# Optimization experiments

Hardware: AMD Instinct MI355X
Metric: run time of the kernel (lower is better)

Reference implementation:

```python
import jax, jax.numpy as jnp
import numpy as np

N = 50000
E = 800000
IN_DIM = 128
HID = 128
OUT_DIM = 64


def _xavier(key, fan_in, fan_out):
    # matches nn.init.xavier_uniform_ on a (out, in) weight
    limit = float(np.sqrt(6.0 / (fan_in + fan_out)))
    return jax.random.uniform(key, (fan_in, fan_out), jnp.float32, -limit, limit)


def setup_inputs() -> dict:
    key = jax.random.key(0)
    ks = jax.random.split(key, 7)
    X = jax.random.normal(ks[0], (N, IN_DIM), jnp.float32)
    edge_row = jax.random.randint(ks[1], (E,), 0, N, jnp.int32)
    edge_col = jax.random.randint(ks[2], (E,), 0, N, jnp.int32)
    edge_weight = jax.random.uniform(ks[3], (E,), jnp.float32)
    W1 = _xavier(ks[4], IN_DIM, HID)
    b1 = jnp.zeros((HID,), jnp.float32)
    W2 = _xavier(ks[5], HID, HID)
    b2 = jnp.zeros((HID,), jnp.float32)
    W3 = _xavier(ks[6], HID, OUT_DIM)
    b3 = jnp.zeros((OUT_DIM,), jnp.float32)
    return {"X": X, "edge_row": edge_row, "edge_col": edge_col,
            "edge_weight": edge_weight,
            "W1": W1, "b1": b1, "W2": W2, "b2": b2, "W3": W3, "b3": b3}


def _spmm(edge_row, edge_col, edge_weight, H):
    # sparse A @ H via gather + segment_sum (COO SpMM)
    msgs = edge_weight[:, None] * H[edge_col]  # [E, d]
    return jax.ops.segment_sum(msgs, edge_row, num_segments=N)


def reference(X, edge_row, edge_col, edge_weight, W1, b1, W2, b2, W3, b3):
    # layer 1: SpMM -> linear -> relu (dropout disabled: eval mode)
    h = _spmm(edge_row, edge_col, edge_weight, X)
    h = jax.nn.relu(h @ W1 + b1)
    # layer 2
    h = _spmm(edge_row, edge_col, edge_weight, h)
    h = jax.nn.relu(h @ W2 + b2)
    # layer 3 (no activation)
    h = _spmm(edge_row, edge_col, edge_weight, h)
    return h @ W3 + b3
```

## Files before the change

kernel.cpp:

```cpp
#include <hip/hip_runtime.h>
#include <hip/hip_fp16.h>


typedef unsigned int uint32;
typedef _Float16 f16x8 __attribute__((ext_vector_type(8)));
using f32x4 = __attribute__((ext_vector_type(4))) float;

static constexpr int BCAP = 3072;

static __device__ __forceinline__ unsigned short f2h(float x) {
    return __builtin_bit_cast(unsigned short, (_Float16)x);
}
static __device__ __forceinline__ __half2 u2h2(uint32 u) {
    return __builtin_bit_cast(__half2, u);
}

__global__ __launch_bounds__(256) void prep_kernel(const float* __restrict__ W1,
                                                   const float* __restrict__ W2,
                                                   const float* __restrict__ W3,
                                                   unsigned short* __restrict__ Wt1,
                                                   unsigned short* __restrict__ Wt2,
                                                   unsigned short* __restrict__ Wt3,
                                                   int* __restrict__ bcur, int nb) {
    int gid = blockIdx.x * 256 + threadIdx.x;
    if (gid < nb) bcur[gid] = 0;
    if (gid < 16384) {
        Wt1[gid] = f2h(W1[(gid & 127) * 128 + (gid >> 7)]);
    } else if (gid < 32768) {
        int g = gid - 16384;
        Wt2[g] = f2h(W2[(g & 127) * 128 + (g >> 7)]);
    } else if (gid < 40960) {
        int g = gid - 32768;
        Wt3[g] = f2h(W3[(g & 127) * 64 + (g >> 7)]);
    }
}

__global__ __launch_bounds__(256) void bucket_scatter_kernel(const int* __restrict__ erow,
                                                             const int* __restrict__ ecol,
                                                             const float* __restrict__ ew,
                                                             int* __restrict__ bcur,
                                                             int2* __restrict__ ebuf, int e) {
    __shared__ int hist[512];
    __shared__ int psc[256];
    __shared__ int fixup[512];
    __shared__ int2 stage[4096];
    int t = threadIdx.x;
    hist[t] = 0; hist[t + 256] = 0;
    __syncthreads();
    int base = blockIdx.x * 4096;
    int4 rows[4];
#pragma unroll
    for (int j = 0; j < 4; j++) {
        int idx = base + j * 1024 + t * 4;
        int4 r = make_int4(-1, -1, -1, -1);
        if (idx + 3 < e) {
            r = *reinterpret_cast<const int4*>(&erow[idx]);
        } else {
            if (idx < e)     r.x = erow[idx];
            if (idx + 1 < e) r.y = erow[idx + 1];
            if (idx + 2 < e) r.z = erow[idx + 2];
            if (idx + 3 < e) r.w = erow[idx + 3];
        }
        rows[j] = r;
        if (r.x >= 0) atomicAdd(&hist[r.x >> 7], 1);
        if (r.y >= 0) atomicAdd(&hist[r.y >> 7], 1);
        if (r.z >= 0) atomicAdd(&hist[r.z >> 7], 1);
        if (r.w >= 0) atomicAdd(&hist[r.w >> 7], 1);
    }
    __syncthreads();
    int c0 = hist[2 * t], c1 = hist[2 * t + 1];
    int s = c0 + c1;
    psc[t] = s;
    __syncthreads();
    for (int off = 1; off < 256; off <<= 1) {
        int u = (t >= off) ? psc[t - off] : 0;
        __syncthreads();
        psc[t] += u;
        __syncthreads();
    }
    int lo0 = psc[t] - s;
    int lo1 = lo0 + c0;
    if (c0) fixup[2 * t]     = 2 * t * BCAP       + atomicAdd(&bcur[2 * t], c0)     - lo0;
    if (c1) fixup[2 * t + 1] = (2 * t + 1) * BCAP + atomicAdd(&bcur[2 * t + 1], c1) - lo1;
    __syncthreads();
    hist[2 * t] = lo0; hist[2 * t + 1] = lo1;
    __syncthreads();
#pragma unroll
    for (int j = 0; j < 4; j++) {
        int idx = base + j * 1024 + t * 4;
        int4 r = rows[j];
        int4 c = make_int4(0, 0, 0, 0);
        float4 w = make_float4(0.f, 0.f, 0.f, 0.f);
        if (idx + 3 < e) {
            c = *reinterpret_cast<const int4*>(&ecol[idx]);
            w = *reinterpret_cast<const float4*>(&ew[idx]);
        } else {
            if (idx < e)     { c.x = ecol[idx];     w.x = ew[idx]; }
            if (idx + 1 < e) { c.y = ecol[idx + 1]; w.y = ew[idx + 1]; }
            if (idx + 2 < e) { c.z = ecol[idx + 2]; w.z = ew[idx + 2]; }
            if (idx + 3 < e) { c.w = ecol[idx + 3]; w.w = ew[idx + 3]; }
        }
        if (r.x >= 0) { int b = r.x >> 7; int sl = atomicAdd(&hist[b], 1);
            stage[sl] = make_int2((b << 23) | ((r.x & 127) << 16) | c.x, (int)f2h(w.x)); }
        if (r.y >= 0) { int b = r.y >> 7; int sl = atomicAdd(&hist[b], 1);
            stage[sl] = make_int2((b << 23) | ((r.y & 127) << 16) | c.y, (int)f2h(w.y)); }
        if (r.z >= 0) { int b = r.z >> 7; int sl = atomicAdd(&hist[b], 1);
            stage[sl] = make_int2((b << 23) | ((r.z & 127) << 16) | c.z, (int)f2h(w.z)); }
        if (r.w >= 0) { int b = r.w >> 7; int sl = atomicAdd(&hist[b], 1);
            stage[sl] = make_int2((b << 23) | ((r.w & 127) << 16) | c.w, (int)f2h(w.w)); }
    }
    __syncthreads();
    int ecnt = min(4096, e - base);
    for (int i = t; i < ecnt; i += 256) {
        int2 v = stage[i];
        int b = ((unsigned)v.x) >> 23;
        int gpos = fixup[b] + i;
        if (gpos - b * BCAP < BCAP) ebuf[gpos] = v;
    }
}

__global__ __launch_bounds__(256) void bucket_sort_kernel(const int* __restrict__ bcur,
                                                          const int2* __restrict__ ebuf,
                                                          int* __restrict__ ecsr,
                                                          int* __restrict__ row_ptr,
                                                          int n, int nb) {
    __shared__ int sc[512];
    __shared__ int2 stage[BCAP];
    __shared__ int sorted[BCAP];
    __shared__ int rc[128], rs[128], c2[128];
    int b = blockIdx.x;
    int t = threadIdx.x;
    sc[t]       = (t < nb)       ? min(bcur[t], BCAP)       : 0;
    sc[t + 256] = (t + 256 < nb) ? min(bcur[t + 256], BCAP) : 0;
    if (t < 128) { rc[t] = 0; c2[t] = 0; }
    __syncthreads();
    for (int off = 1; off < 512; off <<= 1) {
        int a0 = (t >= off) ? sc[t - off] : 0;
        int a1 = (t + 256 >= off) ? sc[t + 256 - off] : 0;
        __syncthreads();
        sc[t] += a0; sc[t + 256] += a1;
        __syncthreads();
    }
    int off_b = (b == 0) ? 0 : sc[b - 1];
    int cnt = sc[b] - off_b;
    if (b == 0 && t == 0) row_ptr[n] = sc[nb - 1];
    for (int i = t; i < cnt; i += 256) {
        int2 v = ebuf[b * BCAP + i];
        stage[i] = v;
        atomicAdd(&rc[(v.x >> 16) & 127], 1);
    }
    __syncthreads();
    if (t < 128) rs[t] = rc[t];
    __syncthreads();
    for (int o = 1; o < 128; o <<= 1) {
        int u = 0;
        if (t < 128 && t >= o) u = rs[t - o];
        __syncthreads();
        if (t < 128) rs[t] += u;
        __syncthreads();
    }
    if (t < 128) {
        int gr = b * 128 + t;
        if (gr < n) row_ptr[gr] = off_b + rs[t] - rc[t];
    }
    __syncthreads();
    for (int i = t; i < cnt; i += 256) {
        int2 v = stage[i];
        int r = (v.x >> 16) & 127;
        int pos = rs[r] - rc[r] + atomicAdd(&c2[r], 1);
        sorted[pos] = (v.y << 16) | (v.x & 0xFFFF);
    }
    __syncthreads();
    for (int i = t; i < cnt; i += 256) ecsr[off_b + i] = sorted[i];
}

template <bool AF32, int NOUT>
__global__ __launch_bounds__(256) void gemm_mfma_kernel(const void* __restrict__ Ap,
                                                        const unsigned short* __restrict__ Wt,
                                                        unsigned short* __restrict__ Zh, int n) {
    constexpr int CT = NOUT / 16;
    int wave = threadIdx.x >> 6;
    int lane = threadIdx.x & 63;
    int m0 = blockIdx.x * 64 + wave * 16;
    int r = lane & 15;
    int g = lane >> 4;
    int arow = min(m0 + r, n - 1);
    f32x4 acc[CT] = {};
#pragma unroll
    for (int kt = 0; kt < 4; kt++) {
        int k0 = kt * 32 + g * 8;
        f16x8 a;
        if constexpr (AF32) {
            const float* A = (const float*)Ap;
            float4 x0 = *reinterpret_cast<const float4*>(&A[(size_t)arow * 128 + k0]);
            float4 x1 = *reinterpret_cast<const float4*>(&A[(size_t)arow * 128 + k0 + 4]);
            a[0] = (_Float16)x0.x; a[1] = (_Float16)x0.y;
            a[2] = (_Float16)x0.z; a[3] = (_Float16)x0.w;
            a[4] = (_Float16)x1.x; a[5] = (_Float16)x1.y;
            a[6] = (_Float16)x1.z; a[7] = (_Float16)x1.w;
        } else {
            const unsigned short* A = (const unsigned short*)Ap;
            a = *reinterpret_cast<const f16x8*>(&A[(size_t)arow * 128 + k0]);
        }
#pragma unroll
        for (int c = 0; c < CT; c++) {
            f16x8 bb = *reinterpret_cast<const f16x8*>(&Wt[(size_t)(c * 16 + r) * 128 + k0]);
            acc[c] = __builtin_amdgcn_mfma_f32_16x16x32_f16(a, bb, acc[c], 0, 0, 0);
        }
    }
#pragma unroll
    for (int c = 0; c < CT; c++) {
#pragma unroll
        for (int rr = 0; rr < 4; rr++) {
            int row = m0 + g * 4 + rr;
            if (row < n) Zh[(size_t)row * NOUT + c * 16 + r] = f2h(acc[c][rr]);
        }
    }
}

__global__ __launch_bounds__(256) void spmm128_kernel(const int* __restrict__ row_ptr,
                                                      const int* __restrict__ ecw,
                                                      const unsigned short* __restrict__ Zh,
                                                      const float* __restrict__ bias,
                                                      unsigned short* __restrict__ Hh, int n) {
    int row = (blockIdx.x * 256 + threadIdx.x) >> 6;
    int lane = threadIdx.x & 63;
    if (row >= n) return;
    int beg = row_ptr[row], end = row_ptr[row + 1];
    int deg = end - beg;
    const int grp = lane >> 4;
    const int gl  = lane & 15;
    __half2 acc[4];
#pragma unroll
    for (int j = 0; j < 4; j++) acc[j] = u2h2(0u);
    for (int wb = 0; wb < deg; wb += 64) {
        int rem = deg - wb;
        int mv = (lane < rem) ? ecw[beg + wb + lane] : 0;
        int nc = (min(rem, 64) + 3) >> 2;
        for (int c0 = 0; c0 < nc; c0 += 4) {
            int v0 = __shfl(mv, (c0 + 0) * 4 + grp, 64);
            int v1 = __shfl(mv, (c0 + 1) * 4 + grp, 64);
            int v2 = __shfl(mv, (c0 + 2) * 4 + grp, 64);
            int v3 = __shfl(mv, (c0 + 3) * 4 + grp, 64);
            uint4 z0 = *reinterpret_cast<const uint4*>(&Zh[((size_t)(uint32)(v0 & 0xFFFF) << 7) + (gl << 3)]);
            uint4 z1 = *reinterpret_cast<const uint4*>(&Zh[((size_t)(uint32)(v1 & 0xFFFF) << 7) + (gl << 3)]);
            uint4 z2 = *reinterpret_cast<const uint4*>(&Zh[((size_t)(uint32)(v2 & 0xFFFF) << 7) + (gl << 3)]);
            uint4 z3 = *reinterpret_cast<const uint4*>(&Zh[((size_t)(uint32)(v3 & 0xFFFF) << 7) + (gl << 3)]);
            uint32 s0 = (uint32)v0 >> 16; s0 |= s0 << 16;
            uint32 s1 = (uint32)v1 >> 16; s1 |= s1 << 16;
            uint32 s2 = (uint32)v2 >> 16; s2 |= s2 << 16;
            uint32 s3 = (uint32)v3 >> 16; s3 |= s3 << 16;
            __half2 w0 = u2h2(s0), w1 = u2h2(s1), w2 = u2h2(s2), w3 = u2h2(s3);
            acc[0] = __hfma2(w0, u2h2(z0.x), acc[0]);
            acc[1] = __hfma2(w0, u2h2(z0.y), acc[1]);
            acc[2] = __hfma2(w0, u2h2(z0.z), acc[2]);
            acc[3] = __hfma2(w0, u2h2(z0.w), acc[3]);
            acc[0] = __hfma2(w1, u2h2(z1.x), acc[0]);
            acc[1] = __hfma2(w1, u2h2(z1.y), acc[1]);
            acc[2] = __hfma2(w1, u2h2(z1.z), acc[2]);
            acc[3] = __hfma2(w1, u2h2(z1.w), acc[3]);
            acc[0] = __hfma2(w2, u2h2(z2.x), acc[0]);
            acc[1] = __hfma2(w2, u2h2(z2.y), acc[1]);
            acc[2] = __hfma2(w2, u2h2(z2.z), acc[2]);
            acc[3] = __hfma2(w2, u2h2(z2.w), acc[3]);
            acc[0] = __hfma2(w3, u2h2(z3.x), acc[0]);
            acc[1] = __hfma2(w3, u2h2(z3.y), acc[1]);
            acc[2] = __hfma2(w3, u2h2(z3.z), acc[2]);
            acc[3] = __hfma2(w3, u2h2(z3.w), acc[3]);
        }
    }
#pragma unroll
    for (int j = 0; j < 4; j++) {
        int u = __builtin_bit_cast(int, acc[j]);
        acc[j] = __hadd2(acc[j], __builtin_bit_cast(__half2, __shfl_xor(u, 16, 64)));
        u = __builtin_bit_cast(int, acc[j]);
        acc[j] = __hadd2(acc[j], __builtin_bit_cast(__half2, __shfl_xor(u, 32, 64)));
    }
    if (lane < 16) {
        int d0 = gl << 3;
        float4 b0 = *reinterpret_cast<const float4*>(&bias[d0]);
        float4 b1 = *reinterpret_cast<const float4*>(&bias[d0 + 4]);
        float2 f0 = __half22float2(acc[0]);
        float2 f1 = __half22float2(acc[1]);
        float2 f2 = __half22float2(acc[2]);
        float2 f3 = __half22float2(acc[3]);
        float v0 = fmaxf(f0.x + b0.x, 0.f), v1 = fmaxf(f0.y + b0.y, 0.f);
        float v2 = fmaxf(f1.x + b0.z, 0.f), v3 = fmaxf(f1.y + b0.w, 0.f);
        float v4 = fmaxf(f2.x + b1.x, 0.f), v5 = fmaxf(f2.y + b1.y, 0.f);
        float v6 = fmaxf(f3.x + b1.z, 0.f), v7 = fmaxf(f3.y + b1.w, 0.f);
        uint4 pk;
        pk.x = (uint32)f2h(v0) | ((uint32)f2h(v1) << 16);
        pk.y = (uint32)f2h(v2) | ((uint32)f2h(v3) << 16);
        pk.z = (uint32)f2h(v4) | ((uint32)f2h(v5) << 16);
        pk.w = (uint32)f2h(v6) | ((uint32)f2h(v7) << 16);
        *reinterpret_cast<uint4*>(&Hh[(size_t)row * 128 + d0]) = pk;
    }
}

__global__ __launch_bounds__(256) void spmm64_kernel(const int* __restrict__ row_ptr,
                                                     const int* __restrict__ ecw,
                                                     const unsigned short* __restrict__ Zh,
                                                     const float* __restrict__ bias,
                                                     float* __restrict__ out, int n) {
    int row = (blockIdx.x * 256 + threadIdx.x) >> 6;
    int lane = threadIdx.x & 63;
    if (row >= n) return;
    int beg = row_ptr[row], end = row_ptr[row + 1];
    int deg = end - beg;
    const int grp = lane >> 4;
    const int gl  = lane & 15;
    __half2 acc[2];
    acc[0] = u2h2(0u); acc[1] = u2h2(0u);
    for (int wb = 0; wb < deg; wb += 64) {
        int rem = deg - wb;
        int mv = (lane < rem) ? ecw[beg + wb + lane] : 0;
        int nc = (min(rem, 64) + 3) >> 2;
        for (int c0 = 0; c0 < nc; c0 += 4) {
            int v0 = __shfl(mv, (c0 + 0) * 4 + grp, 64);
            int v1 = __shfl(mv, (c0 + 1) * 4 + grp, 64);
            int v2 = __shfl(mv, (c0 + 2) * 4 + grp, 64);
            int v3 = __shfl(mv, (c0 + 3) * 4 + grp, 64);
            uint2 z0 = *reinterpret_cast<const uint2*>(&Zh[((size_t)(uint32)(v0 & 0xFFFF) << 6) + (gl << 2)]);
            uint2 z1 = *reinterpret_cast<const uint2*>(&Zh[((size_t)(uint32)(v1 & 0xFFFF) << 6) + (gl << 2)]);
            uint2 z2 = *reinterpret_cast<const uint2*>(&Zh[((size_t)(uint32)(v2 & 0xFFFF) << 6) + (gl << 2)]);
            uint2 z3 = *reinterpret_cast<const uint2*>(&Zh[((size_t)(uint32)(v3 & 0xFFFF) << 6) + (gl << 2)]);
            uint32 s0 = (uint32)v0 >> 16; s0 |= s0 << 16;
            uint32 s1 = (uint32)v1 >> 16; s1 |= s1 << 16;
            uint32 s2 = (uint32)v2 >> 16; s2 |= s2 << 16;
            uint32 s3 = (uint32)v3 >> 16; s3 |= s3 << 16;
            acc[0] = __hfma2(u2h2(s0), u2h2(z0.x), acc[0]);
            acc[1] = __hfma2(u2h2(s0), u2h2(z0.y), acc[1]);
            acc[0] = __hfma2(u2h2(s1), u2h2(z1.x), acc[0]);
            acc[1] = __hfma2(u2h2(s1), u2h2(z1.y), acc[1]);
            acc[0] = __hfma2(u2h2(s2), u2h2(z2.x), acc[0]);
            acc[1] = __hfma2(u2h2(s2), u2h2(z2.y), acc[1]);
            acc[0] = __hfma2(u2h2(s3), u2h2(z3.x), acc[0]);
            acc[1] = __hfma2(u2h2(s3), u2h2(z3.y), acc[1]);
        }
    }
#pragma unroll
    for (int j = 0; j < 2; j++) {
        int u = __builtin_bit_cast(int, acc[j]);
        acc[j] = __hadd2(acc[j], __builtin_bit_cast(__half2, __shfl_xor(u, 16, 64)));
        u = __builtin_bit_cast(int, acc[j]);
        acc[j] = __hadd2(acc[j], __builtin_bit_cast(__half2, __shfl_xor(u, 32, 64)));
    }
    if (lane < 16) {
        int d0 = gl << 2;
        float4 b0 = *reinterpret_cast<const float4*>(&bias[d0]);
        float2 f0 = __half22float2(acc[0]);
        float2 f1 = __half22float2(acc[1]);
        float4 v = make_float4(f0.x + b0.x, f0.y + b0.y, f1.x + b0.z, f1.y + b0.w);
        *reinterpret_cast<float4*>(&out[(size_t)row * 64 + d0]) = v;
    }
}

extern "C" void kernel_launch(void* const* d_in, const int* in_sizes, int n_in,
                              void* d_out, int out_size, void* d_ws, size_t ws_size,
                              hipStream_t stream) {
    const float* X    = (const float*)d_in[0];
    const int*   erow = (const int*)d_in[1];
    const int*   ecol = (const int*)d_in[2];
    const float* ew   = (const float*)d_in[3];
    const float* W1   = (const float*)d_in[4];
    const float* b1   = (const float*)d_in[5];
    const float* W2   = (const float*)d_in[6];
    const float* b2   = (const float*)d_in[7];
    const float* W3   = (const float*)d_in[8];
    const float* b3   = (const float*)d_in[9];
    float* out = (float*)d_out;

    const int n = in_sizes[0] / 128;
    const int e = in_sizes[1];
    const int nb = (n + 127) >> 7;

    char* p = (char*)d_ws;
    auto alloc = [&](size_t bytes) {
        void* r = (void*)p;
        p += (bytes + 255) & ~(size_t)255;
        return r;
    };
    int*            row_ptr = (int*)alloc((size_t)(n + 1) * sizeof(int));
    int*            bcur    = (int*)alloc((size_t)nb * sizeof(int));
    int2*           ebuf    = (int2*)alloc((size_t)nb * BCAP * sizeof(int2));
    int*            ecsr    = (int*)alloc((size_t)e * sizeof(int));
    unsigned short* Zh      = (unsigned short*)alloc((size_t)n * 128 * sizeof(unsigned short));
    unsigned short* Hh      = (unsigned short*)alloc((size_t)n * 128 * sizeof(unsigned short));
    unsigned short* Wt1     = (unsigned short*)alloc(128 * 128 * sizeof(unsigned short));
    unsigned short* Wt2     = (unsigned short*)alloc(128 * 128 * sizeof(unsigned short));
    unsigned short* Wt3     = (unsigned short*)alloc(64 * 128 * sizeof(unsigned short));

    const int eb4k = (e + 4095) / 4096;
    const int gemm_grid  = (n + 63) / 64;
    const int spmm_grid  = (n + 3) / 4;

    prep_kernel<<<160, 256, 0, stream>>>(W1, W2, W3, Wt1, Wt2, Wt3, bcur, nb);
    bucket_scatter_kernel<<<eb4k, 256, 0, stream>>>(erow, ecol, ew, bcur, ebuf, e);
    bucket_sort_kernel<<<nb, 256, 0, stream>>>(bcur, ebuf, ecsr, row_ptr, n, nb);

    gemm_mfma_kernel<true, 128><<<gemm_grid, 256, 0, stream>>>(X, Wt1, Zh, n);
    spmm128_kernel<<<spmm_grid, 256, 0, stream>>>(row_ptr, ecsr, Zh, b1, Hh, n);

    gemm_mfma_kernel<false, 128><<<gemm_grid, 256, 0, stream>>>(Hh, Wt2, Zh, n);
    spmm128_kernel<<<spmm_grid, 256, 0, stream>>>(row_ptr, ecsr, Zh, b2, Hh, n);

    gemm_mfma_kernel<false, 64><<<gemm_grid, 256, 0, stream>>>(Hh, Wt3, Zh, n);
    spmm64_kernel<<<spmm_grid, 256, 0, stream>>>(row_ptr, ecsr, Zh, b3, out, n);
}
```

Baseline: 167.9 us.

## Quantize GEMM outputs to per-row int8 and gather int8 in SpMM

The GEMM epilogue now quantizes each output row to int8 with a per-row absmax scale, staged through shared memory for coalesced stores. The SpMM kernels fold that row scale into the edge weight and gather int8 rows instead of fp16. This halves the bytes moved by the random gather that dominates SpMM. Accumulation switches from packed fp16 to fp32, which costs more ALU work per element and adds int8 quantization error.

```diff
diff --git a/kernel.cpp b/kernel.cpp
--- a/kernel.cpp
+++ b/kernel.cpp
@@ -11,8 +11,8 @@
 static __device__ __forceinline__ unsigned short f2h(float x) {
     return __builtin_bit_cast(unsigned short, (_Float16)x);
 }
-static __device__ __forceinline__ __half2 u2h2(uint32 u) {
-    return __builtin_bit_cast(__half2, u);
+static __device__ __forceinline__ float h2f(uint32 u) {
+    return (float)__builtin_bit_cast(_Float16, (unsigned short)(u & 0xFFFF));
 }
 
 __global__ __launch_bounds__(256) void prep_kernel(const float* __restrict__ W1,
@@ -124,26 +124,26 @@
                                                           int* __restrict__ ecsr,
                                                           int* __restrict__ row_ptr,
                                                           int n, int nb) {
-    __shared__ int sc[512];
+    __shared__ int sc_[512];
     __shared__ int2 stage[BCAP];
     __shared__ int sorted[BCAP];
     __shared__ int rc[128], rs[128], c2[128];
     int b = blockIdx.x;
     int t = threadIdx.x;
-    sc[t]       = (t < nb)       ? min(bcur[t], BCAP)       : 0;
-    sc[t + 256] = (t + 256 < nb) ? min(bcur[t + 256], BCAP) : 0;
+    sc_[t]       = (t < nb)       ? min(bcur[t], BCAP)       : 0;
+    sc_[t + 256] = (t + 256 < nb) ? min(bcur[t + 256], BCAP) : 0;
     if (t < 128) { rc[t] = 0; c2[t] = 0; }
     __syncthreads();
     for (int off = 1; off < 512; off <<= 1) {
-        int a0 = (t >= off) ? sc[t - off] : 0;
-        int a1 = (t + 256 >= off) ? sc[t + 256 - off] : 0;
-        __syncthreads();
-        sc[t] += a0; sc[t + 256] += a1;
-        __syncthreads();
-    }
-    int off_b = (b == 0) ? 0 : sc[b - 1];
-    int cnt = sc[b] - off_b;
-    if (b == 0 && t == 0) row_ptr[n] = sc[nb - 1];
+        int a0 = (t >= off) ? sc_[t - off] : 0;
+        int a1 = (t + 256 >= off) ? sc_[t + 256 - off] : 0;
+        __syncthreads();
+        sc_[t] += a0; sc_[t + 256] += a1;
+        __syncthreads();
+    }
+    int off_b = (b == 0) ? 0 : sc_[b - 1];
+    int cnt = sc_[b] - off_b;
+    if (b == 0 && t == 0) row_ptr[n] = sc_[nb - 1];
     for (int i = t; i < cnt; i += 256) {
         int2 v = ebuf[b * BCAP + i];
         stage[i] = v;
@@ -177,8 +177,11 @@
 template <bool AF32, int NOUT>
 __global__ __launch_bounds__(256) void gemm_mfma_kernel(const void* __restrict__ Ap,
                                                         const unsigned short* __restrict__ Wt,
-                                                        unsigned short* __restrict__ Zh, int n) {
+                                                        signed char* __restrict__ Zq,
+                                                        float* __restrict__ sc, int n) {
     constexpr int CT = NOUT / 16;
+    __shared__ __align__(16) signed char tile[4][16 * NOUT];
+    __shared__ float invs[4][16];
     int wave = threadIdx.x >> 6;
     int lane = threadIdx.x & 63;
     int m0 = blockIdx.x * 64 + wave * 16;
@@ -209,18 +212,33 @@
         }
     }
 #pragma unroll
-    for (int c = 0; c < CT; c++) {
-#pragma unroll
-        for (int rr = 0; rr < 4; rr++) {
-            int row = m0 + g * 4 + rr;
-            if (row < n) Zh[(size_t)row * NOUT + c * 16 + r] = f2h(acc[c][rr]);
-        }
-    }
+    for (int rr = 0; rr < 4; rr++) {
+        float m = 0.f;
+#pragma unroll
+        for (int c = 0; c < CT; c++) m = fmaxf(m, fabsf(acc[c][rr]));
+#pragma unroll
+        for (int s = 1; s < 16; s <<= 1) m = fmaxf(m, __shfl_xor(m, s, 64));
+        float qs = (m > 0.f) ? 127.f / m : 0.f;
+#pragma unroll
+        for (int c = 0; c < CT; c++)
+            tile[wave][(g * 4 + rr) * NOUT + c * 16 + r] = (signed char)(int)rintf(acc[c][rr] * qs);
+        if (r == 0) invs[wave][g * 4 + rr] = m * (1.f / 127.f);
+    }
+#pragma unroll
+    for (int off = 0; off < 16 * NOUT; off += 1024) {
+        int o = off + lane * 16;
+        int grow = m0 + o / NOUT;
+        if (grow < n)
+            *reinterpret_cast<uint4*>(&Zq[(size_t)m0 * NOUT + o]) =
+                *reinterpret_cast<const uint4*>(&tile[wave][o]);
+    }
+    if (lane < 16 && m0 + lane < n) sc[m0 + lane] = invs[wave][lane];
 }
 
 __global__ __launch_bounds__(256) void spmm128_kernel(const int* __restrict__ row_ptr,
                                                       const int* __restrict__ ecw,
-                                                      const unsigned short* __restrict__ Zh,
+                                                      const signed char* __restrict__ Zq,
+                                                      const float* __restrict__ sc,
                                                       const float* __restrict__ bias,
                                                       unsigned short* __restrict__ Hh, int n) {
     int row = (blockIdx.x * 256 + threadIdx.x) >> 6;
@@ -230,76 +248,64 @@
     int deg = end - beg;
     const int grp = lane >> 4;
     const int gl  = lane & 15;
-    __half2 acc[4];
-#pragma unroll
-    for (int j = 0; j < 4; j++) acc[j] = u2h2(0u);
+    float acc[8] = {0.f, 0.f, 0.f, 0.f, 0.f, 0.f, 0.f, 0.f};
     for (int wb = 0; wb < deg; wb += 64) {
         int rem = deg - wb;
         int mv = (lane < rem) ? ecw[beg + wb + lane] : 0;
+        float ms = sc[mv & 0xFFFF];
+        float cwf = h2f((uint32)mv >> 16) * ms;
+        int pk = ((int)f2h(cwf) << 16) | (mv & 0xFFFF);
         int nc = (min(rem, 64) + 3) >> 2;
         for (int c0 = 0; c0 < nc; c0 += 4) {
-            int v0 = __shfl(mv, (c0 + 0) * 4 + grp, 64);
-            int v1 = __shfl(mv, (c0 + 1) * 4 + grp, 64);
-            int v2 = __shfl(mv, (c0 + 2) * 4 + grp, 64);
-            int v3 = __shfl(mv, (c0 + 3) * 4 + grp, 64);
-            uint4 z0 = *reinterpret_cast<const uint4*>(&Zh[((size_t)(uint32)(v0 & 0xFFFF) << 7) + (gl << 3)]);
-            uint4 z1 = *reinterpret_cast<const uint4*>(&Zh[((size_t)(uint32)(v1 & 0xFFFF) << 7) + (gl << 3)]);
-            uint4 z2 = *reinterpret_cast<const uint4*>(&Zh[((size_t)(uint32)(v2 & 0xFFFF) << 7) + (gl << 3)]);
-            uint4 z3 = *reinterpret_cast<const uint4*>(&Zh[((size_t)(uint32)(v3 & 0xFFFF) << 7) + (gl << 3)]);
-            uint32 s0 = (uint32)v0 >> 16; s0 |= s0 << 16;
-            uint32 s1 = (uint32)v1 >> 16; s1 |= s1 << 16;
-            uint32 s2 = (uint32)v2 >> 16; s2 |= s2 << 16;
-            uint32 s3 = (uint32)v3 >> 16; s3 |= s3 << 16;
-            __half2 w0 = u2h2(s0), w1 = u2h2(s1), w2 = u2h2(s2), w3 = u2h2(s3);
-            acc[0] = __hfma2(w0, u2h2(z0.x), acc[0]);
-            acc[1] = __hfma2(w0, u2h2(z0.y), acc[1]);
-            acc[2] = __hfma2(w0, u2h2(z0.z), acc[2]);
-            acc[3] = __hfma2(w0, u2h2(z0.w), acc[3]);
-            acc[0] = __hfma2(w1, u2h2(z1.x), acc[0]);
-            acc[1] = __hfma2(w1, u2h2(z1.y), acc[1]);
-            acc[2] = __hfma2(w1, u2h2(z1.z), acc[2]);
-            acc[3] = __hfma2(w1, u2h2(z1.w), acc[3]);
-            acc[0] = __hfma2(w2, u2h2(z2.x), acc[0]);
-            acc[1] = __hfma2(w2, u2h2(z2.y), acc[1]);
-            acc[2] = __hfma2(w2, u2h2(z2.z), acc[2]);
-            acc[3] = __hfma2(w2, u2h2(z2.w), acc[3]);
-            acc[0] = __hfma2(w3, u2h2(z3.x), acc[0]);
-            acc[1] = __hfma2(w3, u2h2(z3.y), acc[1]);
-            acc[2] = __hfma2(w3, u2h2(z3.z), acc[2]);
-            acc[3] = __hfma2(w3, u2h2(z3.w), acc[3]);
-        }
-    }
-#pragma unroll
-    for (int j = 0; j < 4; j++) {
-        int u = __builtin_bit_cast(int, acc[j]);
-        acc[j] = __hadd2(acc[j], __builtin_bit_cast(__half2, __shfl_xor(u, 16, 64)));
-        u = __builtin_bit_cast(int, acc[j]);
-        acc[j] = __hadd2(acc[j], __builtin_bit_cast(__half2, __shfl_xor(u, 32, 64)));
+            int v0 = __shfl(pk, (c0 + 0) * 4 + grp, 64);
+            int v1 = __shfl(pk, (c0 + 1) * 4 + grp, 64);
+            int v2 = __shfl(pk, (c0 + 2) * 4 + grp, 64);
+            int v3 = __shfl(pk, (c0 + 3) * 4 + grp, 64);
+            uint2 z0 = *reinterpret_cast<const uint2*>(&Zq[((size_t)(uint32)(v0 & 0xFFFF) << 7) + (gl << 3)]);
+            uint2 z1 = *reinterpret_cast<const uint2*>(&Zq[((size_t)(uint32)(v1 & 0xFFFF) << 7) + (gl << 3)]);
+            uint2 z2 = *reinterpret_cast<const uint2*>(&Zq[((size_t)(uint32)(v2 & 0xFFFF) << 7) + (gl << 3)]);
+            uint2 z3 = *reinterpret_cast<const uint2*>(&Zq[((size_t)(uint32)(v3 & 0xFFFF) << 7) + (gl << 3)]);
+            float w0 = h2f((uint32)v0 >> 16), w1 = h2f((uint32)v1 >> 16);
+            float w2 = h2f((uint32)v2 >> 16), w3 = h2f((uint32)v3 >> 16);
+#define ACC8(zz, ww)                                                              \
+            acc[0] = fmaf(ww, (float)(signed char)((zz).x & 0xFF), acc[0]);       \
+            acc[1] = fmaf(ww, (float)(signed char)(((zz).x >> 8) & 0xFF), acc[1]);\
+            acc[2] = fmaf(ww, (float)(signed char)(((zz).x >> 16) & 0xFF), acc[2]);\
+            acc[3] = fmaf(ww, (float)(signed char)((zz).x >> 24), acc[3]);        \
+            acc[4] = fmaf(ww, (float)(signed char)((zz).y & 0xFF), acc[4]);       \
+            acc[5] = fmaf(ww, (float)(signed char)(((zz).y >> 8) & 0xFF), acc[5]);\
+            acc[6] = fmaf(ww, (float)(signed char)(((zz).y >> 16) & 0xFF), acc[6]);\
+            acc[7] = fmaf(ww, (float)(signed char)((zz).y >> 24), acc[7]);
+            ACC8(z0, w0) ACC8(z1, w1) ACC8(z2, w2) ACC8(z3, w3)
+#undef ACC8
+        }
+    }
+#pragma unroll
+    for (int j = 0; j < 8; j++) {
+        acc[j] += __shfl_xor(acc[j], 16, 64);
+        acc[j] += __shfl_xor(acc[j], 32, 64);
     }
     if (lane < 16) {
         int d0 = gl << 3;
         float4 b0 = *reinterpret_cast<const float4*>(&bias[d0]);
         float4 b1 = *reinterpret_cast<const float4*>(&bias[d0 + 4]);
-        float2 f0 = __half22float2(acc[0]);
-        float2 f1 = __half22float2(acc[1]);
-        float2 f2 = __half22float2(acc[2]);
-        float2 f3 = __half22float2(acc[3]);
-        float v0 = fmaxf(f0.x + b0.x, 0.f), v1 = fmaxf(f0.y + b0.y, 0.f);
-        float v2 = fmaxf(f1.x + b0.z, 0.f), v3 = fmaxf(f1.y + b0.w, 0.f);
-        float v4 = fmaxf(f2.x + b1.x, 0.f), v5 = fmaxf(f2.y + b1.y, 0.f);
-        float v6 = fmaxf(f3.x + b1.z, 0.f), v7 = fmaxf(f3.y + b1.w, 0.f);
-        uint4 pk;
-        pk.x = (uint32)f2h(v0) | ((uint32)f2h(v1) << 16);
-        pk.y = (uint32)f2h(v2) | ((uint32)f2h(v3) << 16);
-        pk.z = (uint32)f2h(v4) | ((uint32)f2h(v5) << 16);
-        pk.w = (uint32)f2h(v6) | ((uint32)f2h(v7) << 16);
-        *reinterpret_cast<uint4*>(&Hh[(size_t)row * 128 + d0]) = pk;
+        float v0 = fmaxf(acc[0] + b0.x, 0.f), v1 = fmaxf(acc[1] + b0.y, 0.f);
+        float v2 = fmaxf(acc[2] + b0.z, 0.f), v3 = fmaxf(acc[3] + b0.w, 0.f);
+        float v4 = fmaxf(acc[4] + b1.x, 0.f), v5 = fmaxf(acc[5] + b1.y, 0.f);
+        float v6 = fmaxf(acc[6] + b1.z, 0.f), v7 = fmaxf(acc[7] + b1.w, 0.f);
+        uint4 pk2;
+        pk2.x = (uint32)f2h(v0) | ((uint32)f2h(v1) << 16);
+        pk2.y = (uint32)f2h(v2) | ((uint32)f2h(v3) << 16);
+        pk2.z = (uint32)f2h(v4) | ((uint32)f2h(v5) << 16);
+        pk2.w = (uint32)f2h(v6) | ((uint32)f2h(v7) << 16);
+        *reinterpret_cast<uint4*>(&Hh[(size_t)row * 128 + d0]) = pk2;
     }
 }
 
 __global__ __launch_bounds__(256) void spmm64_kernel(const int* __restrict__ row_ptr,
                                                      const int* __restrict__ ecw,
-                                                     const unsigned short* __restrict__ Zh,
+                                                     const signed char* __restrict__ Zq,
+                                                     const float* __restrict__ sc,
                                                      const float* __restrict__ bias,
                                                      float* __restrict__ out, int n) {
     int row = (blockIdx.x * 256 + threadIdx.x) >> 6;
@@ -309,48 +315,43 @@
     int deg = end - beg;
     const int grp = lane >> 4;
     const int gl  = lane & 15;
-    __half2 acc[2];
-    acc[0] = u2h2(0u); acc[1] = u2h2(0u);
+    float acc[4] = {0.f, 0.f, 0.f, 0.f};
     for (int wb = 0; wb < deg; wb += 64) {
         int rem = deg - wb;
         int mv = (lane < rem) ? ecw[beg + wb + lane] : 0;
+        float ms = sc[mv & 0xFFFF];
+        float cwf = h2f((uint32)mv >> 16) * ms;
+        int pk = ((int)f2h(cwf) << 16) | (mv & 0xFFFF);
         int nc = (min(rem, 64) + 3) >> 2;
         for (int c0 = 0; c0 < nc; c0 += 4) {
-            int v0 = __shfl(mv, (c0 + 0) * 4 + grp, 64);
-            int v1 = __shfl(mv, (c0 + 1) * 4 + grp, 64);
-            int v2 = __shfl(mv, (c0 + 2) * 4 + grp, 64);
-            int v3 = __shfl(mv, (c0 + 3) * 4 + grp, 64);
-            uint2 z0 = *reinterpret_cast<const uint2*>(&Zh[((size_t)(uint32)(v0 & 0xFFFF) << 6) + (gl << 2)]);
-            uint2 z1 = *reinterpret_cast<const uint2*>(&Zh[((size_t)(uint32)(v1 & 0xFFFF) << 6) + (gl << 2)]);
-            uint2 z2 = *reinterpret_cast<const uint2*>(&Zh[((size_t)(uint32)(v2 & 0xFFFF) << 6) + (gl << 2)]);
-            uint2 z3 = *reinterpret_cast<const uint2*>(&Zh[((size_t)(uint32)(v3 & 0xFFFF) << 6) + (gl << 2)]);
-            uint32 s0 = (uint32)v0 >> 16; s0 |= s0 << 16;
-            uint32 s1 = (uint32)v1 >> 16; s1 |= s1 << 16;
-            uint32 s2 = (uint32)v2 >> 16; s2 |= s2 << 16;
-            uint32 s3 = (uint32)v3 >> 16; s3 |= s3 << 16;
-            acc[0] = __hfma2(u2h2(s0), u2h2(z0.x), acc[0]);
-            acc[1] = __hfma2(u2h2(s0), u2h2(z0.y), acc[1]);
-            acc[0] = __hfma2(u2h2(s1), u2h2(z1.x), acc[0]);
-            acc[1] = __hfma2(u2h2(s1), u2h2(z1.y), acc[1]);
-            acc[0] = __hfma2(u2h2(s2), u2h2(z2.x), acc[0]);
-            acc[1] = __hfma2(u2h2(s2), u2h2(z2.y), acc[1]);
-            acc[0] = __hfma2(u2h2(s3), u2h2(z3.x), acc[0]);
-            acc[1] = __hfma2(u2h2(s3), u2h2(z3.y), acc[1]);
-        }
-    }
-#pragma unroll
-    for (int j = 0; j < 2; j++) {
-        int u = __builtin_bit_cast(int, acc[j]);
-        acc[j] = __hadd2(acc[j], __builtin_bit_cast(__half2, __shfl_xor(u, 16, 64)));
-        u = __builtin_bit_cast(int, acc[j]);
-        acc[j] = __hadd2(acc[j], __builtin_bit_cast(__half2, __shfl_xor(u, 32, 64)));
+            int v0 = __shfl(pk, (c0 + 0) * 4 + grp, 64);
+            int v1 = __shfl(pk, (c0 + 1) * 4 + grp, 64);
+            int v2 = __shfl(pk, (c0 + 2) * 4 + grp, 64);
+            int v3 = __shfl(pk, (c0 + 3) * 4 + grp, 64);
+            uint32 z0 = *reinterpret_cast<const uint32*>(&Zq[((size_t)(uint32)(v0 & 0xFFFF) << 6) + (gl << 2)]);
+            uint32 z1 = *reinterpret_cast<const uint32*>(&Zq[((size_t)(uint32)(v1 & 0xFFFF) << 6) + (gl << 2)]);
+            uint32 z2 = *reinterpret_cast<const uint32*>(&Zq[((size_t)(uint32)(v2 & 0xFFFF) << 6) + (gl << 2)]);
+            uint32 z3 = *reinterpret_cast<const uint32*>(&Zq[((size_t)(uint32)(v3 & 0xFFFF) << 6) + (gl << 2)]);
+            float w0 = h2f((uint32)v0 >> 16), w1 = h2f((uint32)v1 >> 16);
+            float w2 = h2f((uint32)v2 >> 16), w3 = h2f((uint32)v3 >> 16);
+#define ACC4(zz, ww)                                                          \
+            acc[0] = fmaf(ww, (float)(signed char)((zz) & 0xFF), acc[0]);     \
+            acc[1] = fmaf(ww, (float)(signed char)(((zz) >> 8) & 0xFF), acc[1]);\
+            acc[2] = fmaf(ww, (float)(signed char)(((zz) >> 16) & 0xFF), acc[2]);\
+            acc[3] = fmaf(ww, (float)(signed char)((zz) >> 24), acc[3]);
+            ACC4(z0, w0) ACC4(z1, w1) ACC4(z2, w2) ACC4(z3, w3)
+#undef ACC4
+        }
+    }
+#pragma unroll
+    for (int j = 0; j < 4; j++) {
+        acc[j] += __shfl_xor(acc[j], 16, 64);
+        acc[j] += __shfl_xor(acc[j], 32, 64);
     }
     if (lane < 16) {
         int d0 = gl << 2;
         float4 b0 = *reinterpret_cast<const float4*>(&bias[d0]);
-        float2 f0 = __half22float2(acc[0]);
-        float2 f1 = __half22float2(acc[1]);
-        float4 v = make_float4(f0.x + b0.x, f0.y + b0.y, f1.x + b0.z, f1.y + b0.w);
+        float4 v = make_float4(acc[0] + b0.x, acc[1] + b0.y, acc[2] + b0.z, acc[3] + b0.w);
         *reinterpret_cast<float4*>(&out[(size_t)row * 64 + d0]) = v;
     }
 }
@@ -384,7 +385,8 @@
     int*            bcur    = (int*)alloc((size_t)nb * sizeof(int));
     int2*           ebuf    = (int2*)alloc((size_t)nb * BCAP * sizeof(int2));
     int*            ecsr    = (int*)alloc((size_t)e * sizeof(int));
-    unsigned short* Zh      = (unsigned short*)alloc((size_t)n * 128 * sizeof(unsigned short));
+    signed char*    Zq      = (signed char*)alloc((size_t)n * 128);
+    float*          scl     = (float*)alloc((size_t)n * sizeof(float));
     unsigned short* Hh      = (unsigned short*)alloc((size_t)n * 128 * sizeof(unsigned short));
     unsigned short* Wt1     = (unsigned short*)alloc(128 * 128 * sizeof(unsigned short));
     unsigned short* Wt2     = (unsigned short*)alloc(128 * 128 * sizeof(unsigned short));
@@ -398,12 +400,12 @@
     bucket_scatter_kernel<<<eb4k, 256, 0, stream>>>(erow, ecol, ew, bcur, ebuf, e);
     bucket_sort_kernel<<<nb, 256, 0, stream>>>(bcur, ebuf, ecsr, row_ptr, n, nb);
 
-    gemm_mfma_kernel<true, 128><<<gemm_grid, 256, 0, stream>>>(X, Wt1, Zh, n);
-    spmm128_kernel<<<spmm_grid, 256, 0, stream>>>(row_ptr, ecsr, Zh, b1, Hh, n);
-
-    gemm_mfma_kernel<false, 128><<<gemm_grid, 256, 0, stream>>>(Hh, Wt2, Zh, n);
-    spmm128_kernel<<<spmm_grid, 256, 0, stream>>>(row_ptr, ecsr, Zh, b2, Hh, n);
-
-    gemm_mfma_kernel<false, 64><<<gemm_grid, 256, 0, stream>>>(Hh, Wt3, Zh, n);
-    spmm64_kernel<<<spmm_grid, 256, 0, stream>>>(row_ptr, ecsr, Zh, b3, out, n);
-}
+    gemm_mfma_kernel<true, 128><<<gemm_grid, 256, 0, stream>>>(X, Wt1, Zq, scl, n);
+    spmm128_kernel<<<spmm_grid, 256, 0, stream>>>(row_ptr, ecsr, Zq, scl, b1, Hh, n);
+
+    gemm_mfma_kernel<false, 128><<<gemm_grid, 256, 0, stream>>>(Hh, Wt2, Zq, scl, n);
+    spmm128_kernel<<<spmm_grid, 256, 0, stream>>>(row_ptr, ecsr, Zq, scl, b2, Hh, n);
+
+    gemm_mfma_kernel<false, 64><<<gemm_grid, 256, 0, stream>>>(Hh, Wt3, Zq, scl, n);
+    spmm64_kernel<<<spmm_grid, 256, 0, stream>>>(row_ptr, ecsr, Zq, scl, b3, out, n);
+}
```

New measurement: 161.9 us. -3.6%, faster.
